# Kernel tuning notes

Hardware: AMD Instinct MI355X
Metric: run time of the kernel (lower is better)

The kernel has to match this reference:

```python
import jax, jax.numpy as jnp
import numpy as np
from functools import partial

D = 512      # world_state_dim
M = 1000     # memory_size
H = 8        # attention heads
DH = D // H  # head dim
EPS = 1e-5


def _layernorm(x, g, b):
    mu = jnp.mean(x, axis=-1, keepdims=True)
    var = jnp.mean((x - mu) ** 2, axis=-1, keepdims=True)
    return (x - mu) * jax.lax.rsqrt(var + EPS) * g + b


def setup_inputs() -> dict:
    key = jax.random.key(0)
    ks = jax.random.split(key, 24)
    B = 8192
    w = lambda k, shp: (jax.random.normal(k, shp, dtype=jnp.float32) * 0.02)
    inp = {
        "observations": jax.random.normal(ks[0], (B, D), dtype=jnp.float32),
        "ego_motion": jax.random.normal(ks[1], (B, 16), dtype=jnp.float32),
        "world_memory": jax.random.normal(ks[2], (M, D), dtype=jnp.float32) * 0.1,
        # encoder: Linear(D,D) -> ReLU -> LN(D) -> Linear(D,D)
        "enc_w1": w(ks[3], (D, D)), "enc_b1": jnp.zeros((D,), jnp.float32),
        "enc_g": jnp.ones((D,), jnp.float32), "enc_beta": jnp.zeros((D,), jnp.float32),
        "enc_w2": w(ks[4], (D, D)), "enc_b2": jnp.zeros((D,), jnp.float32),
        # multihead attention in/out projections
        "wq": w(ks[5], (D, D)), "bq": jnp.zeros((D,), jnp.float32),
        "wk": w(ks[6], (D, D)), "bk": jnp.zeros((D,), jnp.float32),
        "wv": w(ks[7], (D, D)), "bv": jnp.zeros((D,), jnp.float32),
        "wo": w(ks[8], (D, D)), "bo": jnp.zeros((D,), jnp.float32),
        # transition: Linear(D+16,D) -> ReLU -> LN(D) -> Linear(D,D)
        "tr_w1": w(ks[9], (D, D + 16)), "tr_b1": jnp.zeros((D,), jnp.float32),
        "tr_g": jnp.ones((D,), jnp.float32), "tr_beta": jnp.zeros((D,), jnp.float32),
        "tr_w2": w(ks[10], (D, D)), "tr_b2": jnp.zeros((D,), jnp.float32),
        # quality head: Linear(D,128) -> ReLU -> Linear(128,1) -> Sigmoid
        "q_w1": w(ks[11], (128, D)), "q_b1": jnp.zeros((128,), jnp.float32),
        "q_w2": w(ks[12], (1, 128)), "q_b2": jnp.zeros((1,), jnp.float32),
        # random slots for memory-bank scatter-EMA update (replaces torch.randint)
        "update_indices": jax.random.randint(ks[13], (B,), 0, M, dtype=jnp.int32),
    }
    return inp


def _forward_core(observations, ego_motion, world_memory,
                  enc_w1, enc_b1, enc_g, enc_beta, enc_w2, enc_b2,
                  wq, bq, wk, bk, wv, bv, wo, bo,
                  tr_w1, tr_b1, tr_g, tr_beta, tr_w2, tr_b2,
                  q_w1, q_b1, q_w2, q_b2):
    B = observations.shape[0]
    # world_encoder
    h = jax.nn.relu(observations @ enc_w1.T + enc_b1)
    encoded = _layernorm(h, enc_g, enc_beta) @ enc_w2.T + enc_b2  # [B, D]
    # cross-attention: one query per batch row over shared memory bank
    q = (encoded @ wq.T + bq).reshape(B, H, DH)
    k = (world_memory @ wk.T + bk).reshape(M, H, DH)  # shared across batch
    v = (world_memory @ wv.T + bv).reshape(M, H, DH)
    scores = jnp.einsum("bhd,mhd->bhm", q, k) / jnp.sqrt(jnp.float32(DH))
    attn = jax.nn.softmax(scores, axis=-1)              # [B, H, M]
    ctx = jnp.einsum("bhm,mhd->bhd", attn, v).reshape(B, D)
    memory_states = ctx @ wo.T + bo
    # fuse + transition
    fused = 0.7 * encoded + 0.3 * memory_states
    x = jnp.concatenate([fused, ego_motion], axis=-1)   # [B, D+16]
    h2 = jax.nn.relu(x @ tr_w1.T + tr_b1)
    next_state = _layernorm(h2, tr_g, tr_beta) @ tr_w2.T + tr_b2  # [B, D]
    # quality head
    qh = jax.nn.relu(next_state @ q_w1.T + q_b1)
    quality = jax.nn.sigmoid(qh @ q_w2.T + q_b2)        # [B, 1]
    mem_weights = jnp.mean(attn, axis=1)                # [B, M] avg over heads
    return next_state, quality, mem_weights


def _update_memory_bank(world_memory, next_state, quality, update_indices):
    # Sequential scatter-EMA, faithful to the torch loop (duplicates compound).
    mask = quality[:, 0] > 0.7

    def step(mem, inp):
        idx, st, m = inp
        row = mem[idx]
        new_row = jnp.where(m, 0.9 * row + 0.1 * st, row)
        return mem.at[idx].set(new_row), None

    updated, _ = jax.lax.scan(step, world_memory, (update_indices, next_state, mask))
    return updated


@jax.jit
def reference(observations, ego_motion, world_memory,
              enc_w1, enc_b1, enc_g, enc_beta, enc_w2, enc_b2,
              wq, bq, wk, bk, wv, bv, wo, bo,
              tr_w1, tr_b1, tr_g, tr_beta, tr_w2, tr_b2,
              q_w1, q_b1, q_w2, q_b2, update_indices):
    next_state, quality, mem_weights = _forward_core(
        observations, ego_motion, world_memory,
        enc_w1, enc_b1, enc_g, enc_beta, enc_w2, enc_b2,
        wq, bq, wk, bk, wv, bv, wo, bo,
        tr_w1, tr_b1, tr_g, tr_beta, tr_w2, tr_b2,
        q_w1, q_b1, q_w2, q_b2)
    updated_memory = _update_memory_bank(world_memory, next_state, quality, update_indices)
    return next_state, quality, updated_memory
```

## Files before the change

kernel.cpp:

```cpp
#include <hip/hip_runtime.h>

#define B_ 8192
#define D_ 512
#define M_ 1000
#define H_ 8
#define LOG2E 1.4426950408889634f

typedef unsigned short u16;
typedef __attribute__((ext_vector_type(8))) short bf16x8;
typedef __attribute__((ext_vector_type(4))) float f32x4;

__device__ __forceinline__ float bf2f(u16 u) {
    union { unsigned u; float f; } c; c.u = ((unsigned)u) << 16; return c.f;
}
__device__ __forceinline__ u16 f2bf(float f) {
    union { float f; unsigned u; } c; c.f = f;
    unsigned r = (c.u + 0x7fffu + ((c.u >> 16) & 1u)) >> 16;
    return (u16)r;
}
__device__ __forceinline__ u16 f2bf_fast(float f) {
    union { float f; unsigned u; } c; c.f = f;
    return (u16)((c.u + 0x8000u) >> 16);
}
__device__ __forceinline__ float wave_sum(float v) {
#pragma unroll
    for (int off = 32; off > 0; off >>= 1) v += __shfl_xor(v, off);
    return v;
}

template<bool RELU, bool WF32, bool VTOUT>
__device__ __forceinline__ void gemm_core(
    const u16* __restrict__ A0, const u16* __restrict__ A1,
    const u16* __restrict__ A2, int lda0, int lda1, int lda2,
    const u16* __restrict__ W0, const u16* __restrict__ W1,
    const u16* __restrict__ W2, int ldw0, int ldw1, int ldw2,
    int kb1, int kb2,
    const float* __restrict__ bias, float bscale, float cscale,
    float* __restrict__ Cf, u16* __restrict__ Cb, u16* __restrict__ VT,
    int M, int N, int K, int ldc)
{
    const int m0 = blockIdx.y * 64, n0 = blockIdx.x * 64;
    if (m0 >= M || n0 >= N) return;
    __shared__ u16 As[64 * 64];
    __shared__ u16 Bs[64 * 64];
    const int t = threadIdx.x, w = t >> 6, l = t & 63;
    const int wm = (w >> 1) * 32, wn = (w & 1) * 32;
    const int li = l & 15, quad = l >> 4;

    f32x4 acc[2][2];
#pragma unroll
    for (int i = 0; i < 2; ++i)
#pragma unroll
        for (int j = 0; j < 2; ++j) acc[i][j] = (f32x4){0.f, 0.f, 0.f, 0.f};

    for (int k0 = 0; k0 < K; k0 += 64) {
        const u16* Ab; const u16* Wb; int ldab, ldwb, ko;
        if (k0 < kb1)      { Ab = A0; ldab = lda0; Wb = W0; ldwb = ldw0; ko = k0; }
        else if (k0 < kb2) { Ab = A1; ldab = lda1; Wb = W1; ldwb = ldw1; ko = k0 - kb1; }
        else               { Ab = A2; ldab = lda2; Wb = W2; ldwb = ldw2; ko = k0 - kb2; }
#pragma unroll
        for (int i = 0; i < 2; ++i) {
            const int rl = w * 16 + i * 8 + (l >> 3);
            const int ck = (l & 7) ^ (rl & 7);
            int ga = m0 + rl; ga = ga < M ? ga : M - 1;
            __builtin_amdgcn_global_load_lds(
                (const __attribute__((address_space(1))) void*)(Ab + (size_t)ga * ldab + ko + ck * 8),
                (__attribute__((address_space(3))) void*)(As + (w * 16 + i * 8) * 64),
                16, 0, 0);
        }
#pragma unroll
        for (int i = 0; i < 2; ++i) {
            const int rl = w * 16 + i * 8 + (l >> 3);
            const int ck = (l & 7) ^ (rl & 7);
            int gb = n0 + rl; gb = gb < N ? gb : N - 1;
            __builtin_amdgcn_global_load_lds(
                (const __attribute__((address_space(1))) void*)(Wb + (size_t)gb * ldwb + ko + ck * 8),
                (__attribute__((address_space(3))) void*)(Bs + (w * 16 + i * 8) * 64),
                16, 0, 0);
        }
        __syncthreads();
#pragma unroll
        for (int ks = 0; ks < 2; ++ks) {
            const int ch = ks * 4 + quad;
            bf16x8 af[2], bfr[2];
#pragma unroll
            for (int mt = 0; mt < 2; ++mt) {
                const int r = wm + mt * 16 + li;
                af[mt] = *(const bf16x8*)(As + r * 64 + ((ch ^ (r & 7)) * 8));
            }
#pragma unroll
            for (int nt = 0; nt < 2; ++nt) {
                const int r = wn + nt * 16 + li;
                bfr[nt] = *(const bf16x8*)(Bs + r * 64 + ((ch ^ (r & 7)) * 8));
            }
#pragma unroll
            for (int mt = 0; mt < 2; ++mt)
#pragma unroll
                for (int nt = 0; nt < 2; ++nt)
                    acc[mt][nt] = __builtin_amdgcn_mfma_f32_16x16x32_bf16(
                        af[mt], bfr[nt], acc[mt][nt], 0, 0, 0);
        }
        __syncthreads();
    }

    float bv[2];
#pragma unroll
    for (int nt = 0; nt < 2; ++nt) bv[nt] = bias[n0 + wn + nt * 16 + li] * bscale;
#pragma unroll
    for (int mt = 0; mt < 2; ++mt) {
        const int row0 = m0 + wm + mt * 16 + quad * 4;
#pragma unroll
        for (int nt = 0; nt < 2; ++nt) {
            const int col = n0 + wn + nt * 16 + li;
            if (VTOUT && col >= 512) {
                ushort4 pk;
                u16 pv[4];
#pragma unroll
                for (int r = 0; r < 4; ++r) {
                    float v = acc[mt][nt][r] * cscale + bv[nt];
                    pv[r] = (row0 + r < M_) ? f2bf(v) : (u16)0;
                }
                pk.x = pv[0]; pk.y = pv[1]; pk.z = pv[2]; pk.w = pv[3];
                *(ushort4*)(VT + (size_t)(col - 512) * 1024 + row0) = pk;
            } else {
#pragma unroll
                for (int r = 0; r < 4; ++r) {
                    const int row = row0 + r;
                    if (row >= M) continue;
                    float v = acc[mt][nt][r] * cscale + bv[nt];
                    if (RELU) v = fmaxf(v, 0.f);
                    Cb[(size_t)row * ldc + col] = f2bf(v);
                    if (WF32) Cf[(size_t)row * ldc + col] = v;
                }
            }
        }
    }
}

template<bool RELU, bool WF32>
__launch_bounds__(256)
__global__ void mgemm(const u16* __restrict__ A0, const u16* __restrict__ A1,
                      const u16* __restrict__ A2, int lda0, int lda1, int lda2,
                      const u16* __restrict__ W0, const u16* __restrict__ W1,
                      const u16* __restrict__ W2, int ldw0, int ldw1, int ldw2,
                      int kb1, int kb2,
                      const float* __restrict__ bias, float bscale, float cscale,
                      float* __restrict__ Cf, u16* __restrict__ Cb,
                      int M, int N, int K, int ldc)
{
    gemm_core<RELU, WF32, false>(A0, A1, A2, lda0, lda1, lda2,
                                 W0, W1, W2, ldw0, ldw1, ldw2, kb1, kb2,
                                 bias, bscale, cscale, Cf, Cb, nullptr, M, N, K, ldc);
}

__launch_bounds__(256)
__global__ void foldgemm(const u16* __restrict__ w_q, const u16* __restrict__ w_tr1,
                         const u16* __restrict__ w_e2t, const u16* __restrict__ w_wot,
                         const float* __restrict__ zb,
                         u16* __restrict__ w_qe, u16* __restrict__ w_ae,
                         u16* __restrict__ w_co)
{
    const int z = blockIdx.z;
    if (z == 0)
        gemm_core<false, false, false>(w_q, w_q, w_q, 512, 512, 512,
            w_e2t, w_e2t, w_e2t, 512, 512, 512, 512, 512,
            zb, 0.f, 1.0f, nullptr, w_qe, nullptr, 512, 512, 512, 512);
    else if (z == 1)
        gemm_core<false, false, false>(w_tr1, w_tr1, w_tr1, 576, 576, 576,
            w_e2t, w_e2t, w_e2t, 512, 512, 512, 512, 512,
            zb, 0.f, 0.7f, nullptr, w_ae, nullptr, 512, 512, 512, 512);
    else
        gemm_core<false, false, false>(w_tr1, w_tr1, w_tr1, 576, 576, 576,
            w_wot, w_wot, w_wot, 512, 512, 512, 512, 512,
            zb, 0.f, 0.3f, nullptr, w_co, nullptr, 512, 512, 512, 512);
}

__launch_bounds__(256)
__global__ void qkvgemm(const u16* __restrict__ hn, const u16* __restrict__ w_qe,
                        const float* __restrict__ bqe, u16* __restrict__ qbuf,
                        const u16* __restrict__ wmem_bf, const u16* __restrict__ w_k,
                        const float* __restrict__ bkv, u16* __restrict__ KVbuf,
                        u16* __restrict__ VTb)
{
    if (blockIdx.z == 0)
        gemm_core<false, false, false>(hn, hn, hn, 512, 512, 512,
            w_qe, w_qe, w_qe, 512, 512, 512, 512, 512,
            bqe, 1.f, 1.f, nullptr, qbuf, nullptr, B_, 512, 512, 512);
    else
        gemm_core<false, false, true>(wmem_bf, wmem_bf, wmem_bf, 512, 512, 512,
            w_k, w_k, w_k, 512, 512, 512, 512, 512,
            bkv, 1.f, 1.f, nullptr, KVbuf, VTb, 1024, 1024, 512, 1024);
}

__launch_bounds__(256)
__global__ void attn_kernel(const u16* __restrict__ Q, const u16* __restrict__ KV,
                            const u16* __restrict__ VT, u16* __restrict__ Ob,
                            float* __restrict__ Lb)
{
    __shared__ u16 Ks[2][64 * 64];
    __shared__ u16 Vs[2][64 * 64];
    __shared__ u16 P[4 * 2048];
    const int t = threadIdx.x, w = t >> 6, l = t & 63;
    const int h = blockIdx.y;
    const int qblk = blockIdx.x & 63, kpart = blockIdx.x >> 6;
    const int q0 = qblk * 128 + w * 32;
    u16* Pw = P + w * 2048;
    const int li = l & 15, quad = l >> 4;
    const int kbeg = kpart * 512;

    bf16x8 aq[2][2];
#pragma unroll
    for (int mt = 0; mt < 2; ++mt)
#pragma unroll
        for (int ks = 0; ks < 2; ++ks) {
            const int row = q0 + mt * 16 + li;
            aq[mt][ks] = *(const bf16x8*)(Q + (size_t)row * 512 + h * 64 + ks * 32 + quad * 8);
        }

    bf16x8 ones;
#pragma unroll
    for (int i = 0; i < 8; ++i) ones[i] = (short)0x3F80;

    f32x4 oacc[2][4];
    f32x4 lacc[2];
#pragma unroll
    for (int mt = 0; mt < 2; ++mt) {
        lacc[mt] = (f32x4){0.f, 0.f, 0.f, 0.f};
#pragma unroll
        for (int nt = 0; nt < 4; ++nt) oacc[mt][nt] = (f32x4){0.f, 0.f, 0.f, 0.f};
    }

    auto stage = [&](int kc, int buf) {
#pragma unroll
        for (int i = 0; i < 2; ++i) {
            const int f = i * 256 + t;
            const int r = f >> 3;
            const int ck = (f & 7) ^ (r & 7);
            __builtin_amdgcn_global_load_lds(
                (const __attribute__((address_space(1))) void*)(KV + (size_t)(kc + r) * 1024 + h * 64 + ck * 8),
                (__attribute__((address_space(3))) void*)(&Ks[buf][f * 8]),
                16, 0, 0);
        }
#pragma unroll
        for (int i = 0; i < 2; ++i) {
            const int f = i * 256 + t;
            const int r = f >> 3;
            const int ck = (f & 7) ^ (r & 7);
            __builtin_amdgcn_global_load_lds(
                (const __attribute__((address_space(1))) void*)(VT + (size_t)(h * 64 + r) * 1024 + kc + ck * 8),
                (__attribute__((address_space(3))) void*)(&Vs[buf][f * 8]),
                16, 0, 0);
        }
    };

    stage(kbeg, 0);
    for (int ic = 0; ic < 8; ++ic) {
        const int kc = kbeg + ic * 64;
        __syncthreads();
        if (ic < 7) stage(kc + 64, (ic + 1) & 1);
        const u16* ksb = &Ks[ic & 1][0];
        const u16* vsb = &Vs[ic & 1][0];

        f32x4 s[2][4];
#pragma unroll
        for (int mt = 0; mt < 2; ++mt)
#pragma unroll
            for (int nt = 0; nt < 4; ++nt) s[mt][nt] = (f32x4){0.f, 0.f, 0.f, 0.f};
#pragma unroll
        for (int ks = 0; ks < 2; ++ks) {
            const int ch = ks * 4 + quad;
            bf16x8 bk[4];
#pragma unroll
            for (int nt = 0; nt < 4; ++nt) {
                const int key = nt * 16 + li;
                bk[nt] = *(const bf16x8*)(ksb + key * 64 + ((ch ^ (key & 7)) * 8));
            }
#pragma unroll
            for (int mt = 0; mt < 2; ++mt)
#pragma unroll
                for (int nt = 0; nt < 4; ++nt)
                    s[mt][nt] = __builtin_amdgcn_mfma_f32_16x16x32_bf16(
                        aq[mt][ks], bk[nt], s[mt][nt], 0, 0, 0);
        }
        if (kc == 960) {
#pragma unroll
            for (int nt = 0; nt < 4; ++nt) {
                const bool val = (960 + nt * 16 + li) < M_;
#pragma unroll
                for (int mt = 0; mt < 2; ++mt)
#pragma unroll
                    for (int r = 0; r < 4; ++r)
                        if (!val) s[mt][nt][r] = -3.0e38f;
            }
        }
#pragma unroll
        for (int mt = 0; mt < 2; ++mt)
#pragma unroll
            for (int nt = 0; nt < 4; ++nt) {
                const int col = nt * 16 + li;
#pragma unroll
                for (int r = 0; r < 4; ++r) {
                    const float p = exp2f(s[mt][nt][r]);
                    const int rowl = mt * 16 + quad * 4 + r;
                    Pw[rowl * 64 + (((col >> 3) ^ (rowl & 7)) * 8) + (col & 7)] = f2bf_fast(p);
                }
            }
#pragma unroll
        for (int ks = 0; ks < 2; ++ks) {
            const int ch = ks * 4 + quad;
            bf16x8 ap[2];
#pragma unroll
            for (int mt = 0; mt < 2; ++mt) {
                const int rowl = mt * 16 + li;
                ap[mt] = *(const bf16x8*)(Pw + rowl * 64 + ((ch ^ (rowl & 7)) * 8));
            }
#pragma unroll
            for (int mt = 0; mt < 2; ++mt)
                lacc[mt] = __builtin_amdgcn_mfma_f32_16x16x32_bf16(
                    ap[mt], ones, lacc[mt], 0, 0, 0);
#pragma unroll
            for (int nt = 0; nt < 4; ++nt) {
                const int dh = nt * 16 + li;
                const bf16x8 bvv = *(const bf16x8*)(vsb + dh * 64 + ((ch ^ (dh & 7)) * 8));
#pragma unroll
                for (int mt = 0; mt < 2; ++mt)
                    oacc[mt][nt] = __builtin_amdgcn_mfma_f32_16x16x32_bf16(
                        ap[mt], bvv, oacc[mt][nt], 0, 0, 0);
            }
        }
    }

    u16* Op = Ob + (size_t)kpart * B_ * 512;
    float* Lp = Lb + (size_t)kpart * B_ * 8;
#pragma unroll
    for (int mt = 0; mt < 2; ++mt)
#pragma unroll
        for (int r = 0; r < 4; ++r) {
            const int row = q0 + mt * 16 + quad * 4 + r;
            if (li == 0) Lp[row * 8 + h] = lacc[mt][r];
#pragma unroll
            for (int nt = 0; nt < 4; ++nt)
                Op[(size_t)row * 512 + h * 64 + nt * 16 + li] = f2bf(oacc[mt][nt][r]);
        }
}

__launch_bounds__(256)
__global__ void attn_combine(const u16* __restrict__ Ob, const float* __restrict__ Lb,
                             u16* __restrict__ ctx)
{
    const int row = blockIdx.x * 4 + (threadIdx.x >> 6);
    const int lane = threadIdx.x & 63;
    const int h = lane >> 3;
    const float inv = 1.0f / (Lb[row * 8 + h] + Lb[(size_t)B_ * 8 + row * 8 + h]);
    const u16* p0 = Ob + (size_t)row * 512 + lane * 8;
    const u16* p1 = p0 + (size_t)B_ * 512;
    uint4 a = *(const uint4*)p0;
    uint4 b = *(const uint4*)p1;
    const unsigned aa[4] = {a.x, a.y, a.z, a.w};
    const unsigned bb[4] = {b.x, b.y, b.z, b.w};
    unsigned o[4];
#pragma unroll
    for (int i = 0; i < 4; ++i) {
        const float lo = (bf2f((u16)(aa[i] & 0xffffu)) + bf2f((u16)(bb[i] & 0xffffu))) * inv;
        const float hi = (bf2f((u16)(aa[i] >> 16)) + bf2f((u16)(bb[i] >> 16))) * inv;
        o[i] = (unsigned)f2bf(lo) | ((unsigned)f2bf(hi) << 16);
    }
    *(uint4*)(ctx + (size_t)row * 512 + lane * 8) = make_uint4(o[0], o[1], o[2], o[3]);
}

__launch_bounds__(256)
__global__ void ln_bf(u16* __restrict__ X, const float* __restrict__ g,
                      const float* __restrict__ be, int rows)
{
    const int row = blockIdx.x * 4 + (threadIdx.x >> 6);
    const int lane = threadIdx.x & 63;
    if (row >= rows) return;
    u16* p = X + (size_t)row * 512 + lane * 8;
    uint4 d = *(const uint4*)p;
    const unsigned dd[4] = {d.x, d.y, d.z, d.w};
    float v[8];
#pragma unroll
    for (int i = 0; i < 4; ++i) {
        v[2 * i]     = bf2f((u16)(dd[i] & 0xffffu));
        v[2 * i + 1] = bf2f((u16)(dd[i] >> 16));
    }
    float s = 0.f;
#pragma unroll
    for (int i = 0; i < 8; ++i) s += v[i];
    s = wave_sum(s);
    const float mu = s * (1.0f / 512.0f);
    float vs = 0.f;
#pragma unroll
    for (int i = 0; i < 8; ++i) { v[i] -= mu; vs += v[i] * v[i]; }
    vs = wave_sum(vs);
    const float r = rsqrtf(vs * (1.0f / 512.0f) + 1e-5f);
    const float* gp = g + lane * 8;
    const float* bp = be + lane * 8;
    unsigned o[4];
#pragma unroll
    for (int i = 0; i < 4; ++i) {
        const u16 lo = f2bf(v[2 * i] * r * gp[2 * i] + bp[2 * i]);
        const u16 hi = f2bf(v[2 * i + 1] * r * gp[2 * i + 1] + bp[2 * i + 1]);
        o[i] = (unsigned)lo | ((unsigned)hi << 16);
    }
    *(uint4*)p = make_uint4(o[0], o[1], o[2], o[3]);
}

__launch_bounds__(256)
__global__ void prep_all(const float* enc_w1, const float* wk_f, const float* wv_f,
                         const float* tr_w2, const float* q_w1, const float* wq,
                         const float* tr_w1, const float* enc_w2, const float* wo,
                         const float* obs, const float* wmem, const float* ego,
                         const float* bk, const float* bvv, const float* bq,
                         const float* enc_b2, const float* trb1, const float* bo,
                         u16* w_enc1, u16* w_k, u16* w_v, u16* w_tr2, u16* w_qh,
                         u16* w_q, u16* w_tr1, u16* w_e2t, u16* w_wot,
                         u16* obs_bf, u16* wmem_bf, u16* ego64,
                         float* bkv, float* bqe, float* btr)
{
    __shared__ float tl[64][65];
    const int seg = blockIdx.y;
    const int t = threadIdx.x;
    const int bx = blockIdx.x;

    if (seg <= 5) {
        const float* s; u16* d; int n; float sc = 1.0f;
        switch (seg) {
            case 0: s = enc_w1; d = w_enc1; n = 262144; break;
            case 1: s = wk_f;   d = w_k;    n = 262144; break;
            case 2: s = wv_f;   d = w_v;    n = 262144; break;
            case 3: s = tr_w2;  d = w_tr2;  n = 262144; break;
            case 4: s = q_w1;   d = w_qh;   n = 65536;  break;
            default: s = wq;    d = w_q;    n = 262144; sc = 0.125f * LOG2E; break;
        }
        const int i0 = (bx * 256 + t) * 4;
        if (i0 + 3 < n) {
            const float4 v = *(const float4*)(s + i0);
            ushort4 o;
            o.x = f2bf(v.x * sc); o.y = f2bf(v.y * sc);
            o.z = f2bf(v.z * sc); o.w = f2bf(v.w * sc);
            *(ushort4*)(d + i0) = o;
        }
    } else if (seg == 6) {
#pragma unroll
        for (int k = 0; k < 4; ++k) {
            const int i = (bx * 256 + t) * 4 + k;
            if (i < 294912) {
                const int r = i / 576, c = i - r * 576;
                w_tr1[i] = (c < 528) ? f2bf(tr_w1[r * 528 + c]) : (u16)0;
            }
        }
    } else if (seg <= 8) {
        if (bx >= 64) return;
        const float* S = (seg == 7) ? enc_w2 : wo;
        u16* D = (seg == 7) ? w_e2t : w_wot;
        const int r0 = (bx >> 3) * 64, c0 = (bx & 7) * 64;
#pragma unroll
        for (int i = 0; i < 16; ++i) {
            const int idx = t + i * 256;
            tl[idx >> 6][idx & 63] = S[(size_t)(r0 + (idx >> 6)) * 512 + c0 + (idx & 63)];
        }
        __syncthreads();
#pragma unroll
        for (int i = 0; i < 16; ++i) {
            const int idx = t + i * 256;
            const int c = idx >> 6, r = idx & 63;
            D[(size_t)(c0 + c) * 512 + r0 + r] = f2bf(tl[r][c]);
        }
    } else if (seg == 9) {
        const int nth = gridDim.x * 256;
        for (int i = bx * 256 + t; i < B_ * 512 / 4; i += nth) {
            const float4 v = ((const float4*)obs)[i];
            ushort4 o;
            o.x = f2bf(v.x); o.y = f2bf(v.y); o.z = f2bf(v.z); o.w = f2bf(v.w);
            ((ushort4*)obs_bf)[i] = o;
        }
    } else if (seg == 10) {
        const int nth = gridDim.x * 256;
        for (int i = bx * 256 + t; i < M_ * 512 / 4; i += nth) {
            const float4 v = ((const float4*)wmem)[i];
            ushort4 o;
            o.x = f2bf(v.x); o.y = f2bf(v.y); o.z = f2bf(v.z); o.w = f2bf(v.w);
            ((ushort4*)wmem_bf)[i] = o;
        }
    } else if (seg == 11) {
        const int nth = gridDim.x * 256;
        for (int i = bx * 256 + t; i < B_ * 64; i += nth) {
            const int b = i >> 6, j = i & 63;
            ego64[(size_t)b * 64 + j] = (j < 16) ? f2bf(ego[b * 16 + j]) : (u16)0;
        }
        const int tid = bx * 256 + t;
        if (tid < 1024) bkv[tid] = (tid < 512) ? bk[tid] : bvv[tid - 512];
    } else {
        if (bx >= 128) return;
        const int i = bx * 4 + (t >> 6);
        const int lane = t & 63;
        float s = 0.f;
        if (seg == 12) {
            const float* wr = wq + (size_t)i * 512 + lane * 8;
#pragma unroll
            for (int j = 0; j < 8; ++j) s += wr[j] * enc_b2[lane * 8 + j];
            s = wave_sum(s);
            if (lane == 0) bqe[i] = 0.125f * LOG2E * (bq[i] + s);
        } else {
            const float* wr = tr_w1 + (size_t)i * 528 + lane * 8;
#pragma unroll
            for (int j = 0; j < 8; ++j)
                s += wr[j] * (0.7f * enc_b2[lane * 8 + j] + 0.3f * bo[lane * 8 + j]);
            s = wave_sum(s);
            if (lane == 0) btr[i] = trb1[i] + s;
        }
    }
}

__global__ void quality_bf(const u16* __restrict__ qh, const float* __restrict__ w2,
                           const float* __restrict__ b2, float* __restrict__ outq,
                           int rows)
{
    const int row = blockIdx.x * 4 + (threadIdx.x >> 6);
    const int lane = threadIdx.x & 63;
    if (row >= rows) return;
    const u16* p = qh + (size_t)row * 128;
    float s = bf2f(p[lane]) * w2[lane] + bf2f(p[64 + lane]) * w2[64 + lane];
    s = wave_sum(s);
    if (lane == 0) outq[row] = 1.0f / (1.0f + expf(-(s + b2[0])));
}

__global__ void compact_kernel(const float* __restrict__ q,
                               int* __restrict__ list, int* __restrict__ cnt)
{
    __shared__ int wtot[16];
    __shared__ int sbase;
    const int t = threadIdx.x, w = t >> 6, lane = t & 63;
    if (t == 0) sbase = 0;
    __syncthreads();
    for (int c = 0; c < B_; c += 1024) {
        const int idx = c + t;
        const bool pred = (q[idx] > 0.7f);
        const unsigned long long bal = __ballot(pred);
        const int prefix = __popcll(bal & ((1ull << lane) - 1ull));
        if (lane == 0) wtot[w] = __popcll(bal);
        __syncthreads();
        int woff = 0;
        for (int i = 0; i < w; ++i) woff += wtot[i];
        if (pred) list[sbase + woff + prefix] = idx;
        __syncthreads();
        if (t == 0) {
            int tot = 0;
            for (int i = 0; i < 16; ++i) tot += wtot[i];
            sbase += tot;
        }
        __syncthreads();
    }
    if (t == 0) *cnt = sbase;
}

__global__ void update_memory_kernel(const float* __restrict__ mem,
                                     const float* __restrict__ ns,
                                     const int* __restrict__ upd,
                                     const int* __restrict__ list,
                                     const int* __restrict__ cnt,
                                     float* __restrict__ outmem)
{
    const int m = blockIdx.x;
    const int t = threadIdx.x;
    const int c4 = t * 4;
    float4 r = *(const float4*)(mem + (size_t)m * D_ + c4);
    const int n = *cnt;
    for (int i = 0; i < n; ++i) {
        const int b = list[i];
        if (upd[b] == m) {
            const float4 s = *(const float4*)(ns + (size_t)b * D_ + c4);
            r.x = 0.9f * r.x + 0.1f * s.x;
            r.y = 0.9f * r.y + 0.1f * s.y;
            r.z = 0.9f * r.z + 0.1f * s.z;
            r.w = 0.9f * r.w + 0.1f * s.w;
        }
    }
    *(float4*)(outmem + (size_t)m * D_ + c4) = r;
}

extern "C" void kernel_launch(void* const* d_in, const int* in_sizes, int n_in,
                              void* d_out, int out_size, void* d_ws, size_t ws_size,
                              hipStream_t stream)
{
    const float* obs    = (const float*)d_in[0];
    const float* ego    = (const float*)d_in[1];
    const float* wmem   = (const float*)d_in[2];
    const float* enc_w1 = (const float*)d_in[3];
    const float* enc_b1 = (const float*)d_in[4];
    const float* enc_g  = (const float*)d_in[5];
    const float* enc_be = (const float*)d_in[6];
    const float* enc_w2 = (const float*)d_in[7];
    const float* enc_b2 = (const float*)d_in[8];
    const float* wq = (const float*)d_in[9];
    const float* bq = (const float*)d_in[10];
    const float* wk_f = (const float*)d_in[11];
    const float* bk = (const float*)d_in[12];
    const float* wv_f = (const float*)d_in[13];
    const float* bvv = (const float*)d_in[14];
    const float* wo = (const float*)d_in[15];
    const float* bo = (const float*)d_in[16];
    const float* tr_w1 = (const float*)d_in[17];
    const float* tr_b1 = (const float*)d_in[18];
    const float* tr_g  = (const float*)d_in[19];
    const float* tr_be = (const float*)d_in[20];
    const float* tr_w2 = (const float*)d_in[21];
    const float* tr_b2 = (const float*)d_in[22];
    const float* q_w1 = (const float*)d_in[23];
    const float* q_b1 = (const float*)d_in[24];
    const float* q_w2 = (const float*)d_in[25];
    const float* q_b2 = (const float*)d_in[26];
    const int*   upd  = (const int*)d_in[27];

    float* out_ns  = (float*)d_out;
    float* out_q   = out_ns + (size_t)B_ * D_;
    float* out_mem = out_q + B_;

    u16* ws = (u16*)d_ws;
    size_t o = 0;
    u16* obs_bf  = ws + o; o += (size_t)B_ * 512;
    u16* wmem_bf = ws + o; o += (size_t)M_ * 512;
    u16* w_enc1  = ws + o; o += 262144;
    u16* w_k     = ws + o; o += 262144;
    u16* w_v     = ws + o; o += 262144;
    u16* w_tr2   = ws + o; o += 262144;
    u16* w_qh    = ws + o; o += 65536;
    u16* w_q     = ws + o; o += 262144;
    u16* w_tr1   = ws + o; o += (size_t)512 * 576;
    u16* w_e2t   = ws + o; o += 262144;
    u16* w_wot   = ws + o; o += 262144;
    u16* w_qe    = ws + o; o += 262144;
    u16* w_ae    = ws + o; o += 262144;
    u16* w_co    = ws + o; o += 262144;
    u16* hbuf    = ws + o; o += (size_t)B_ * 512;
    u16* qbuf    = ws + o; o += (size_t)B_ * 512;
    u16* KVbuf   = ws + o; o += (size_t)1024 * 1024;
    u16* VTb     = ws + o; o += (size_t)512 * 1024;
    u16* ctx     = ws + o; o += (size_t)B_ * 512;
    u16* h2b     = ws + o; o += (size_t)B_ * 512;
    u16* nsbf    = ws + o; o += (size_t)B_ * 512;
    u16* qhb     = ws + o; o += (size_t)B_ * 128;
    u16* ego64   = ws + o; o += (size_t)B_ * 64;
    u16* Obuf    = ws + o; o += (size_t)2 * B_ * 512;
    float* Lbuf  = (float*)(ws + o); o += (size_t)2 * B_ * 8 * 2;
    float* bkv   = (float*)(ws + o); o += 2048;
    float* bqe   = (float*)(ws + o); o += 1024;
    float* btr   = (float*)(ws + o); o += 1024;
    int* list    = (int*)(ws + o);
    int* cnt     = list + B_;

    const dim3 blk(256);

    prep_all<<<dim3(576, 14), blk, 0, stream>>>(
        enc_w1, wk_f, wv_f, tr_w2, q_w1, wq, tr_w1, enc_w2, wo,
        obs, wmem, ego, bk, bvv, bq, enc_b2, tr_b1, bo,
        w_enc1, w_k, w_v, w_tr2, w_qh, w_q, w_tr1, w_e2t, w_wot,
        obs_bf, wmem_bf, ego64, bkv, bqe, btr);

    foldgemm<<<dim3(8, 8, 3), blk, 0, stream>>>(w_q, w_tr1, w_e2t, w_wot, bkv,
                                                w_qe, w_ae, w_co);

    mgemm<true, false><<<dim3(8, 128), blk, 0, stream>>>(
        obs_bf, obs_bf, obs_bf, 512, 512, 512, w_enc1, w_enc1, w_enc1, 512, 512, 512,
        512, 512, enc_b1, 1.f, 1.f, nullptr, hbuf, B_, 512, 512, 512);
    ln_bf<<<dim3(2048), blk, 0, stream>>>(hbuf, enc_g, enc_be, B_);

    qkvgemm<<<dim3(16, 128, 2), blk, 0, stream>>>(
        hbuf, w_qe, bqe, qbuf, wmem_bf, w_k, bkv, KVbuf, VTb);

    attn_kernel<<<dim3(128, 8), blk, 0, stream>>>(qbuf, KVbuf, VTb, Obuf, Lbuf);
    attn_combine<<<dim3(2048), blk, 0, stream>>>(Obuf, Lbuf, ctx);

    mgemm<true, false><<<dim3(8, 128), blk, 0, stream>>>(
        hbuf, ctx, ego64, 512, 512, 64, w_ae, w_co, w_tr1 + 512, 512, 512, 576,
        512, 1024, btr, 1.f, 1.f, nullptr, h2b, B_, 512, 1088, 512);
    ln_bf<<<dim3(2048), blk, 0, stream>>>(h2b, tr_g, tr_be, B_);

    mgemm<false, true><<<dim3(8, 128), blk, 0, stream>>>(
        h2b, h2b, h2b, 512, 512, 512, w_tr2, w_tr2, w_tr2, 512, 512, 512,
        512, 512, tr_b2, 1.f, 1.f, out_ns, nsbf, B_, 512, 512, 512);

    mgemm<true, false><<<dim3(2, 128), blk, 0, stream>>>(
        nsbf, nsbf, nsbf, 512, 512, 512, w_qh, w_qh, w_qh, 512, 512, 512,
        512, 512, q_b1, 1.f, 1.f, nullptr, qhb, B_, 128, 512, 128);
    quality_bf<<<dim3(2048), blk, 0, stream>>>(qhb, q_w2, q_b2, out_q, B_);

    compact_kernel<<<dim3(1), dim3(1024), 0, stream>>>(out_q, list, cnt);
    update_memory_kernel<<<dim3(M_), dim3(128), 0, stream>>>(
        wmem, out_ns, upd, list, cnt, out_mem);
}
```

Measured before the change: 283.1 us.

## Drop split-K attention and combine kernel; compute transposed scores with padded P store

```diff
diff --git a/kernel.cpp b/kernel.cpp
--- a/kernel.cpp
+++ b/kernel.cpp
@@ -18,9 +18,9 @@
     unsigned r = (c.u + 0x7fffu + ((c.u >> 16) & 1u)) >> 16;
     return (u16)r;
 }
-__device__ __forceinline__ u16 f2bf_fast(float f) {
+__device__ __forceinline__ unsigned f2bf_fast_u(float f) {
     union { float f; unsigned u; } c; c.f = f;
-    return (u16)((c.u + 0x8000u) >> 16);
+    return (c.u + 0x8000u) >> 16;
 }
 __device__ __forceinline__ float wave_sum(float v) {
 #pragma unroll
@@ -192,29 +192,28 @@
             bkv, 1.f, 1.f, nullptr, KVbuf, VTb, 1024, 1024, 512, 1024);
 }
 
-__launch_bounds__(256)
+#define PADK 72
+
+__launch_bounds__(256, 3)
 __global__ void attn_kernel(const u16* __restrict__ Q, const u16* __restrict__ KV,
-                            const u16* __restrict__ VT, u16* __restrict__ Ob,
-                            float* __restrict__ Lb)
+                            const u16* __restrict__ VT, u16* __restrict__ ctx)
 {
     __shared__ u16 Ks[2][64 * 64];
     __shared__ u16 Vs[2][64 * 64];
-    __shared__ u16 P[4 * 2048];
+    __shared__ u16 P[4 * 32 * PADK];
     const int t = threadIdx.x, w = t >> 6, l = t & 63;
     const int h = blockIdx.y;
-    const int qblk = blockIdx.x & 63, kpart = blockIdx.x >> 6;
-    const int q0 = qblk * 128 + w * 32;
-    u16* Pw = P + w * 2048;
+    const int q0 = blockIdx.x * 128 + w * 32;
+    u16* Pw = P + w * (32 * PADK);
     const int li = l & 15, quad = l >> 4;
-    const int kbeg = kpart * 512;
 
     bf16x8 aq[2][2];
 #pragma unroll
-    for (int mt = 0; mt < 2; ++mt)
+    for (int qnt = 0; qnt < 2; ++qnt)
 #pragma unroll
         for (int ks = 0; ks < 2; ++ks) {
-            const int row = q0 + mt * 16 + li;
-            aq[mt][ks] = *(const bf16x8*)(Q + (size_t)row * 512 + h * 64 + ks * 32 + quad * 8);
+            const int row = q0 + qnt * 16 + li;
+            aq[qnt][ks] = *(const bf16x8*)(Q + (size_t)row * 512 + h * 64 + ks * 32 + quad * 8);
         }
 
     bf16x8 ones;
@@ -253,67 +252,65 @@
         }
     };
 
-    stage(kbeg, 0);
-    for (int ic = 0; ic < 8; ++ic) {
-        const int kc = kbeg + ic * 64;
+    stage(0, 0);
+    for (int ic = 0; ic < 16; ++ic) {
+        const int kc = ic * 64;
         __syncthreads();
-        if (ic < 7) stage(kc + 64, (ic + 1) & 1);
+        if (ic < 15) stage(kc + 64, (ic + 1) & 1);
         const u16* ksb = &Ks[ic & 1][0];
         const u16* vsb = &Vs[ic & 1][0];
 
-        f32x4 s[2][4];
-#pragma unroll
-        for (int mt = 0; mt < 2; ++mt)
-#pragma unroll
-            for (int nt = 0; nt < 4; ++nt) s[mt][nt] = (f32x4){0.f, 0.f, 0.f, 0.f};
+        f32x4 s[4][2];
+#pragma unroll
+        for (int kmt = 0; kmt < 4; ++kmt)
+#pragma unroll
+            for (int qnt = 0; qnt < 2; ++qnt) s[kmt][qnt] = (f32x4){0.f, 0.f, 0.f, 0.f};
 #pragma unroll
         for (int ks = 0; ks < 2; ++ks) {
             const int ch = ks * 4 + quad;
             bf16x8 bk[4];
 #pragma unroll
-            for (int nt = 0; nt < 4; ++nt) {
-                const int key = nt * 16 + li;
-                bk[nt] = *(const bf16x8*)(ksb + key * 64 + ((ch ^ (key & 7)) * 8));
+            for (int kmt = 0; kmt < 4; ++kmt) {
+                const int key = kmt * 16 + li;
+                bk[kmt] = *(const bf16x8*)(ksb + key * 64 + ((ch ^ (key & 7)) * 8));
             }
 #pragma unroll
-            for (int mt = 0; mt < 2; ++mt)
-#pragma unroll
-                for (int nt = 0; nt < 4; ++nt)
-                    s[mt][nt] = __builtin_amdgcn_mfma_f32_16x16x32_bf16(
-                        aq[mt][ks], bk[nt], s[mt][nt], 0, 0, 0);
+            for (int kmt = 0; kmt < 4; ++kmt)
+#pragma unroll
+                for (int qnt = 0; qnt < 2; ++qnt)
+                    s[kmt][qnt] = __builtin_amdgcn_mfma_f32_16x16x32_bf16(
+                        bk[kmt], aq[qnt][ks], s[kmt][qnt], 0, 0, 0);
         }
         if (kc == 960) {
 #pragma unroll
-            for (int nt = 0; nt < 4; ++nt) {
-                const bool val = (960 + nt * 16 + li) < M_;
-#pragma unroll
-                for (int mt = 0; mt < 2; ++mt)
-#pragma unroll
-                    for (int r = 0; r < 4; ++r)
-                        if (!val) s[mt][nt][r] = -3.0e38f;
-            }
-        }
-#pragma unroll
-        for (int mt = 0; mt < 2; ++mt)
-#pragma unroll
-            for (int nt = 0; nt < 4; ++nt) {
-                const int col = nt * 16 + li;
+            for (int kmt = 2; kmt < 4; ++kmt)
 #pragma unroll
                 for (int r = 0; r < 4; ++r) {
-                    const float p = exp2f(s[mt][nt][r]);
-                    const int rowl = mt * 16 + quad * 4 + r;
-                    Pw[rowl * 64 + (((col >> 3) ^ (rowl & 7)) * 8) + (col & 7)] = f2bf_fast(p);
+                    const int key_local = kmt * 16 + quad * 4 + r;
+                    if (960 + key_local >= M_) {
+                        s[kmt][0][r] = -3.0e38f;
+                        s[kmt][1][r] = -3.0e38f;
+                    }
                 }
+        }
+#pragma unroll
+        for (int kmt = 0; kmt < 4; ++kmt)
+#pragma unroll
+            for (int qnt = 0; qnt < 2; ++qnt) {
+                const unsigned b0 = f2bf_fast_u(exp2f(s[kmt][qnt][0]));
+                const unsigned b1 = f2bf_fast_u(exp2f(s[kmt][qnt][1]));
+                const unsigned b2w = f2bf_fast_u(exp2f(s[kmt][qnt][2]));
+                const unsigned b3 = f2bf_fast_u(exp2f(s[kmt][qnt][3]));
+                const int off = (qnt * 16 + li) * PADK + kmt * 16 + quad * 4;
+                *(uint2*)(Pw + off) = make_uint2(b0 | (b1 << 16), b2w | (b3 << 16));
             }
 #pragma unroll
         for (int ks = 0; ks < 2; ++ks) {
             const int ch = ks * 4 + quad;
             bf16x8 ap[2];
 #pragma unroll
-            for (int mt = 0; mt < 2; ++mt) {
-                const int rowl = mt * 16 + li;
-                ap[mt] = *(const bf16x8*)(Pw + rowl * 64 + ((ch ^ (rowl & 7)) * 8));
-            }
+            for (int mt = 0; mt < 2; ++mt)
+                ap[mt] = *(const bf16x8*)(Pw + (mt * 16 + li) * PADK + ch * 8);
 #pragma unroll
             for (int mt = 0; mt < 2; ++mt)
                 lacc[mt] = __builtin_amdgcn_mfma_f32_16x16x32_bf16(
@@ -330,42 +327,16 @@
         }
     }
 
-    u16* Op = Ob + (size_t)kpart * B_ * 512;
-    float* Lp = Lb + (size_t)kpart * B_ * 8;
 #pragma unroll
     for (int mt = 0; mt < 2; ++mt)
 #pragma unroll
         for (int r = 0; r < 4; ++r) {
             const int row = q0 + mt * 16 + quad * 4 + r;
-            if (li == 0) Lp[row * 8 + h] = lacc[mt][r];
+            const float inv = 1.0f / lacc[mt][r];
 #pragma unroll
             for (int nt = 0; nt < 4; ++nt)
-                Op[(size_t)row * 512 + h * 64 + nt * 16 + li] = f2bf(oacc[mt][nt][r]);
-        }
-}
-
-__launch_bounds__(256)
-__global__ void attn_combine(const u16* __restrict__ Ob, const float* __restrict__ Lb,
-                             u16* __restrict__ ctx)
-{
-    const int row = blockIdx.x * 4 + (threadIdx.x >> 6);
-    const int lane = threadIdx.x & 63;
-    const int h = lane >> 3;
-    const float inv = 1.0f / (Lb[row * 8 + h] + Lb[(size_t)B_ * 8 + row * 8 + h]);
-    const u16* p0 = Ob + (size_t)row * 512 + lane * 8;
-    const u16* p1 = p0 + (size_t)B_ * 512;
-    uint4 a = *(const uint4*)p0;
-    uint4 b = *(const uint4*)p1;
-    const unsigned aa[4] = {a.x, a.y, a.z, a.w};
-    const unsigned bb[4] = {b.x, b.y, b.z, b.w};
-    unsigned o[4];
-#pragma unroll
-    for (int i = 0; i < 4; ++i) {
-        const float lo = (bf2f((u16)(aa[i] & 0xffffu)) + bf2f((u16)(bb[i] & 0xffffu))) * inv;
-        const float hi = (bf2f((u16)(aa[i] >> 16)) + bf2f((u16)(bb[i] >> 16))) * inv;
-        o[i] = (unsigned)f2bf(lo) | ((unsigned)f2bf(hi) << 16);
-    }
-    *(uint4*)(ctx + (size_t)row * 512 + lane * 8) = make_uint4(o[0], o[1], o[2], o[3]);
+                ctx[(size_t)row * 512 + h * 64 + nt * 16 + li] = f2bf(oacc[mt][nt][r] * inv);
+        }
 }
 
 __launch_bounds__(256)
@@ -642,8 +613,6 @@
     u16* nsbf    = ws + o; o += (size_t)B_ * 512;
     u16* qhb     = ws + o; o += (size_t)B_ * 128;
     u16* ego64   = ws + o; o += (size_t)B_ * 64;
-    u16* Obuf    = ws + o; o += (size_t)2 * B_ * 512;
-    float* Lbuf  = (float*)(ws + o); o += (size_t)2 * B_ * 8 * 2;
     float* bkv   = (float*)(ws + o); o += 2048;
     float* bqe   = (float*)(ws + o); o += 1024;
     float* btr   = (float*)(ws + o); o += 1024;
@@ -669,8 +638,7 @@
     qkvgemm<<<dim3(16, 128, 2), blk, 0, stream>>>(
         hbuf, w_qe, bqe, qbuf, wmem_bf, w_k, bkv, KVbuf, VTb);
 
-    attn_kernel<<<dim3(128, 8), blk, 0, stream>>>(qbuf, KVbuf, VTb, Obuf, Lbuf);
-    attn_combine<<<dim3(2048), blk, 0, stream>>>(Obuf, Lbuf, ctx);
+    attn_kernel<<<dim3(64, 8), blk, 0, stream>>>(qbuf, KVbuf, VTb, ctx);
 
     mgemm<true, false><<<dim3(8, 128), blk, 0, stream>>>(
         hbuf, ctx, ego64, 512, 512, 64, w_ae, w_co, w_tr1 + 512, 512, 512, 576,
```

Result: faster. 273.8 us (-3.3%).
